# Performance work log

Hardware: AMD Instinct MI355X
Metric: run time of the kernel (lower is better)

The kernel has to match this reference:

```python
import jax, jax.numpy as jnp
import numpy as np

B=64; HW=14; E=2048; L=30; V=10000; EMB=512; AML=768; ADL=500
D=512+ADL   # decoder_dim + article_downlen = 1012
A=512+ADL   # attention_dim + article_downlen = 1012

def setup_inputs() -> dict:
    key = jax.random.key(0)
    ks = jax.random.split(key, 20)
    s = 0.02
    lin = lambda k, i, o: (jax.random.normal(k, (i, o), jnp.float32) * s)
    inp = {}
    inp['encoder_out'] = jax.random.normal(ks[0], (B, HW, HW, E), jnp.float32)
    inp['encoded_captions'] = jax.random.randint(ks[1], (B, L), 0, V)
    cl = jax.random.randint(ks[2], (B, 1), 2, L + 1)
    inp['caption_lengths'] = cl.at[0, 0].set(L)  # ensure max decode length == L-1
    inp['encoded_articles'] = jax.random.normal(ks[3], (B, 1, AML), jnp.float32)
    inp['article_lengths'] = jax.random.randint(ks[4], (B, 1), 1, AML)
    inp['blank_context'] = 0
    inp['E_emb'] = jax.random.uniform(ks[5], (V, EMB), jnp.float32, -0.1, 0.1)
    inp['W_par'] = lin(ks[6], AML, ADL); inp['b_par'] = jnp.zeros(ADL, jnp.float32)
    inp['W_enc'] = lin(ks[7], E, A);     inp['b_enc'] = jnp.zeros(A, jnp.float32)
    inp['W_dec'] = lin(ks[8], D, A);     inp['b_dec'] = jnp.zeros(A, jnp.float32)
    inp['W_full'] = lin(ks[9], A, 1);    inp['b_full'] = jnp.zeros(1, jnp.float32)
    inp['W_h'] = lin(ks[10], E + ADL, D); inp['b_h'] = jnp.zeros(D, jnp.float32)
    inp['W_c'] = lin(ks[11], E + ADL, D); inp['b_c'] = jnp.zeros(D, jnp.float32)
    inp['W_fb'] = lin(ks[12], D, E);      inp['b_fb'] = jnp.zeros(E, jnp.float32)
    inp['W_ih'] = lin(ks[13], EMB + E, 4 * D); inp['b_ih'] = jnp.zeros(4 * D, jnp.float32)
    inp['W_hh'] = lin(ks[14], D, 4 * D);       inp['b_hh'] = jnp.zeros(4 * D, jnp.float32)
    inp['W_fc'] = jax.random.uniform(ks[15], (D, V), jnp.float32, -0.1, 0.1)
    inp['b_fc'] = jnp.zeros(V, jnp.float32)
    return inp

def reference(encoder_out, encoded_captions, caption_lengths, encoded_articles,
              article_lengths, blank_context, E_emb, W_par, b_par, W_enc, b_enc,
              W_dec, b_dec, W_full, b_full, W_h, b_h, W_c, b_c, W_fb, b_fb,
              W_ih, b_ih, W_hh, b_hh, W_fc, b_fc):
    Bv = encoder_out.shape[0]
    enc = encoder_out.reshape(Bv, -1, encoder_out.shape[-1])  # (B, P, E)
    lens = caption_lengths[:, 0]
    sort_ind = jnp.argsort(-lens)
    lens = lens[sort_ind]
    enc = enc[sort_ind]
    caps = encoded_captions[sort_ind]
    arts = encoded_articles[sort_ind]
    emb = E_emb[caps]                                   # (B, L, EMB)
    context = (arts @ W_par + b_par)[:, 0, :]           # ParagraphEncoder -> (B, ADL)
    dec_in = jnp.concatenate([enc.mean(axis=1), context], axis=1)
    h0 = dec_in @ W_h + b_h
    c0 = dec_in @ W_c + b_c
    dlens = lens - 1
    att1 = enc @ W_enc + b_enc                          # loop-invariant, (B, P, A)
    T = emb.shape[1] - 1

    def step(carry, t):
        h, c = carry
        active = (dlens > t)[:, None]                   # prefix mask (sorted desc)
        att2 = h @ W_dec + b_dec
        scores = (jax.nn.relu(att1 + att2[:, None, :]) @ W_full)[..., 0] + b_full[0]
        alpha = jax.nn.softmax(scores, axis=1)          # (B, P)
        awe = jnp.einsum('bp,bpe->be', alpha, enc)
        awe = jax.nn.sigmoid(h @ W_fb + b_fb) * awe     # gated attention encoding
        x = jnp.concatenate([emb[:, t, :], awe], axis=1)
        gates = x @ W_ih + b_ih + h @ W_hh + b_hh       # torch LSTMCell, gate order i,f,g,o
        i, f, g, o = jnp.split(gates, 4, axis=1)
        c_new = jax.nn.sigmoid(f) * c + jax.nn.sigmoid(i) * jnp.tanh(g)
        h_new = jax.nn.sigmoid(o) * jnp.tanh(c_new)
        preds = jnp.where(active, h_new @ W_fc + b_fc, 0.0)
        alpha_m = jnp.where(active, alpha, 0.0)
        h = jnp.where(active, h_new, h)
        c = jnp.where(active, c_new, c)
        return (h, c), (preds, alpha_m)

    _, (preds, alphas) = jax.lax.scan(step, (h0, c0), jnp.arange(T))
    predictions = jnp.transpose(preds, (1, 0, 2))       # (B, T, V)
    alphas = jnp.transpose(alphas, (1, 0, 2))           # (B, T, P)
    return (predictions, caps, dlens, alphas, sort_ind)
```

## Files before the change

kernel.cpp:

```cpp
#include <hip/hip_runtime.h>
#include <math.h>

#define B_   64
#define P_   196
#define E_   2048
#define L_   30
#define T_   29
#define V_   10000
#define EMB_ 512
#define AML_ 768
#define ADL_ 500
#define D_   1012
#define A_   1012
#define G4_  4048
#define XK_  2560

typedef unsigned short u16;
typedef __attribute__((ext_vector_type(8))) short bf16x8;
typedef __attribute__((ext_vector_type(4))) float f32x4;

__device__ __forceinline__ float sigf(float x) { return 1.f / (1.f + __expf(-x)); }
__device__ __forceinline__ float tanhf_fast(float x) { return 1.f - 2.f / (__expf(2.f * x) + 1.f); }
__device__ __forceinline__ u16 f2bf(float f) {
    unsigned u = __float_as_uint(f);
    return (u16)((u + 0x7FFFu + ((u >> 16) & 1u)) >> 16);
}
__device__ __forceinline__ float bf2f(u16 v) { return __uint_as_float(((unsigned)v) << 16); }

__global__ void k_setup(const int* __restrict__ clen, const int* __restrict__ caps,
                        float* __restrict__ out_caps, float* __restrict__ out_dlens,
                        float* __restrict__ out_sind,
                        int* __restrict__ sort_ind, int* __restrict__ dlens_i,
                        int* __restrict__ nact, int* __restrict__ caps_s,
                        int* __restrict__ gcnt)
{
    __shared__ int lens[B_];
    int t = threadIdx.x;
    if (t < B_) lens[t] = clen[t];
    if (t < 64) gcnt[t] = 0;
    __syncthreads();
    if (t < B_) {
        int my = lens[t];
        int rank = 0;
        for (int j = 0; j < B_; ++j) {
            int lj = lens[j];
            if (lj > my || (lj == my && j < t)) rank++;
        }
        sort_ind[rank] = t;
    }
    __syncthreads();
    if (t < B_) {
        int orig = sort_ind[t];
        int dl = lens[orig] - 1;
        dlens_i[t] = dl;
        out_dlens[t] = (float)dl;
        out_sind[t] = (float)orig;
        for (int j = 0; j < L_; ++j) {
            int cv = caps[orig * L_ + j];
            caps_s[t * L_ + j] = cv;
            out_caps[t * L_ + j] = (float)cv;
        }
    }
    __syncthreads();
    if (t < T_) {
        int cnt = 0;
        for (int j = 0; j < B_; ++j) cnt += (dlens_i[j] > t) ? 1 : 0;
        nact[t] = cnt;
    }
}

__global__ void k_zero(float4* __restrict__ p, long n4)
{
    long i = (long)blockIdx.x * 256 + threadIdx.x;
    if (i < n4) p[i] = make_float4(0.f, 0.f, 0.f, 0.f);
}

__global__ void k_cvt_enc(const float* __restrict__ enc, const int* __restrict__ sort_ind,
                          u16* __restrict__ A_bf)
{
    int row = blockIdx.y;
    int b = row / 196, p = row - b * 196;
    int e4 = (blockIdx.x * 256 + threadIdx.x) * 4;
    const float* src = enc + ((long)sort_ind[b] * 196 + p) * E_ + e4;
    float4 v = *(const float4*)src;
    unsigned lo = (unsigned)f2bf(v.x) | ((unsigned)f2bf(v.y) << 16);
    unsigned hi = (unsigned)f2bf(v.z) | ((unsigned)f2bf(v.w) << 16);
    uint2 pk; pk.x = lo; pk.y = hi;
    *(uint2*)(A_bf + (long)row * E_ + e4) = pk;
}

__global__ void k_transpose(const float* __restrict__ src, u16* __restrict__ dst,
                            int K, int N, int Kp, int Np)
{
    __shared__ float tile[32][33];
    int n0 = blockIdx.x * 32, k0 = blockIdx.y * 32;
    int tx = threadIdx.x, ty = threadIdx.y;
    for (int r = ty; r < 32; r += 8) {
        int k = k0 + r, n = n0 + tx;
        tile[r][tx] = (k < K && n < N) ? src[(long)k * N + n] : 0.f;
    }
    __syncthreads();
    for (int r = ty; r < 32; r += 8) {
        int n = n0 + r, k = k0 + tx;
        if (n < Np && k < Kp) dst[(long)n * Kp + k] = f2bf(tile[tx][r]);
    }
}

__global__ void k_encmean(const float* __restrict__ enc, const int* __restrict__ sort_ind,
                          u16* __restrict__ dec_in)
{
    int b = blockIdx.y;
    int e = blockIdx.x * 256 + threadIdx.x;
    int orig = sort_ind[b];
    const float* src = enc + (long)orig * P_ * E_ + e;
    float s = 0.f;
    for (int p = 0; p < P_; ++p) s += src[(long)p * E_];
    dec_in[(long)b * XK_ + e] = f2bf(s * (1.f / 196.f));
}

__global__ void k_ctx(const float* __restrict__ arts, const float* __restrict__ W_par,
                      const float* __restrict__ b_par, const int* __restrict__ sort_ind,
                      u16* __restrict__ dec_in)
{
    int b = blockIdx.y;
    int k = blockIdx.x * 256 + threadIdx.x;
    if (k >= 512) return;
    float s = 0.f;
    if (k < ADL_) {
        int orig = sort_ind[b];
        const float* ar = arts + (long)orig * AML_;
        s = b_par[k];
        for (int m = 0; m < AML_; ++m) s = fmaf(ar[m], W_par[m * ADL_ + k], s);
    }
    dec_in[(long)b * XK_ + E_ + k] = f2bf(s);
}

__global__ void k_emb_all(const float* __restrict__ E_emb, const int* __restrict__ caps_s,
                          u16* __restrict__ emb_all)
{
    int t = blockIdx.x;
    int b = blockIdx.y;
    int tok = caps_s[b * L_ + t];
    for (int k = threadIdx.x; k < EMB_; k += 256)
        emb_all[((long)t * B_ + b) * EMB_ + k] = f2bf(E_emb[(long)tok * EMB_ + k]);
}

__global__ void __launch_bounds__(256) k_att1_mfma(
    const u16* __restrict__ A, const u16* __restrict__ W,
    const float* __restrict__ bias, u16* __restrict__ Yb)
{
    int w = threadIdx.x >> 6, lane = threadIdx.x & 63;
    int lr = lane & 15, lk = (lane >> 4) * 8;
    int n0 = blockIdx.x * 256 + w * 64;
    int r0 = blockIdx.y * 64;
    f32x4 acc[4][4];
#pragma unroll
    for (int i = 0; i < 4; ++i)
#pragma unroll
        for (int j = 0; j < 4; ++j) acc[i][j] = (f32x4){0.f, 0.f, 0.f, 0.f};
    const u16* ap = A + (long)(r0 + lr) * E_ + lk;
    const u16* wp = W + (long)(n0 + lr) * E_ + lk;
    for (int k = 0; k < E_; k += 32) {
        bf16x8 af[4], bf[4];
#pragma unroll
        for (int mt = 0; mt < 4; ++mt) af[mt] = *(const bf16x8*)(ap + (long)mt * 16 * E_ + k);
#pragma unroll
        for (int nt = 0; nt < 4; ++nt) bf[nt] = *(const bf16x8*)(wp + (long)nt * 16 * E_ + k);
#pragma unroll
        for (int mt = 0; mt < 4; ++mt)
#pragma unroll
            for (int nt = 0; nt < 4; ++nt)
                acc[mt][nt] = __builtin_amdgcn_mfma_f32_16x16x32_bf16(af[mt], bf[nt], acc[mt][nt], 0, 0, 0);
    }
#pragma unroll
    for (int mt = 0; mt < 4; ++mt) {
#pragma unroll
        for (int nt = 0; nt < 4; ++nt) {
            int n = n0 + nt * 16 + lr;
            float bv = (n < A_) ? bias[n] : 0.f;
#pragma unroll
            for (int j = 0; j < 4; ++j) {
                int row = r0 + mt * 16 + (lane >> 4) * 4 + j;
                u16 outv = (n < A_) ? f2bf(acc[mt][nt][j] + bv) : (u16)0;
                Yb[(long)row * 1024 + n] = outv;
            }
        }
    }
}

template <int ACT, int OUT, int PADZ>
__global__ void __launch_bounds__(256) k_skinny(
    const u16* __restrict__ A1, const u16* __restrict__ W1, int K1,
    const float* __restrict__ bias1, void* __restrict__ Yv,
    long ldY, long offY, int Nmax,
    const int* __restrict__ nact, int t)
{
    int Bact = (t >= 0) ? nact[t] : B_;
    if (Bact <= 0) return;
    int mmax = (Bact + 15) >> 4;
    int w = threadIdx.x >> 6, lane = threadIdx.x & 63;
    int lr = lane & 15, lk = (lane >> 4) * 8;
    int n0 = blockIdx.x * 64 + w * 16;
    f32x4 acc[4];
#pragma unroll
    for (int m = 0; m < 4; ++m) acc[m] = (f32x4){0.f, 0.f, 0.f, 0.f};

    int n = n0 + lr;
    int nc = n < Nmax ? n : Nmax - 1;
    const u16* a1p = A1 + (long)lr * K1 + lk;
    const u16* w1p = W1 + (long)nc * K1 + lk;
    for (int k = 0; k < K1; k += 32) {
        bf16x8 bw = *(const bf16x8*)(w1p + k);
#pragma unroll
        for (int m = 0; m < 4; ++m)
            if (m < mmax) {
                bf16x8 aw = *(const bf16x8*)(a1p + (long)m * 16 * K1 + k);
                acc[m] = __builtin_amdgcn_mfma_f32_16x16x32_bf16(aw, bw, acc[m], 0, 0, 0);
            }
    }
    float bv = (n < Nmax) ? bias1[n] : 0.f;
#pragma unroll
    for (int m = 0; m < 4; ++m) {
        if (m < mmax) {
#pragma unroll
            for (int j = 0; j < 4; ++j) {
                int b = m * 16 + (lane >> 4) * 4 + j;
                if (b < Bact) {
                    float v = acc[m][j] + bv;
                    if (ACT == 1) v = sigf(v);
                    if (n < Nmax) {
                        if (OUT == 1) ((u16*)Yv)[(long)b * ldY + offY + n] = f2bf(v);
                        else          ((float*)Yv)[(long)b * ldY + offY + n] = v;
                    } else if (PADZ) {
                        if (OUT == 1) ((u16*)Yv)[(long)b * ldY + offY + n] = 0;
                        else          ((float*)Yv)[(long)b * ldY + offY + n] = 0.f;
                    }
                }
            }
        }
    }
}

__global__ void __launch_bounds__(256) k_att2fb(
    const u16* __restrict__ h_bf, const u16* __restrict__ WT_dec,
    const u16* __restrict__ WT_fb, const float* __restrict__ b_dec,
    const float* __restrict__ b_fb, float* __restrict__ att2p,
    float* __restrict__ fbp, const int* __restrict__ nact, int t)
{
    int Bact = nact[t];
    if (Bact <= 0) return;
    int mmax = (Bact + 15) >> 4;
    int kh = blockIdx.x / 48;
    int nb = blockIdx.x - kh * 48;
    int isfb = nb >= 16;
    const u16* W = isfb ? WT_fb : WT_dec;
    const float* bias = isfb ? b_fb : b_dec;
    int Nmax = isfb ? E_ : A_;
    int nb2 = isfb ? nb - 16 : nb;
    long ldY = isfb ? (long)E_ : 1024L;
    float* Y = (isfb ? fbp : att2p) + (long)kh * B_ * ldY;

    int w = threadIdx.x >> 6, lane = threadIdx.x & 63;
    int lr = lane & 15, lk = (lane >> 4) * 8;
    int n = nb2 * 64 + w * 16 + lr;
    int nc = n < Nmax ? n : Nmax - 1;
    int k0 = kh * 256;
    f32x4 acc[4];
#pragma unroll
    for (int m = 0; m < 4; ++m) acc[m] = (f32x4){0.f, 0.f, 0.f, 0.f};
    const u16* ap = h_bf + (long)lr * 1024 + k0 + lk;
    const u16* wp = W + (long)nc * 1024 + k0 + lk;
    for (int k = 0; k < 256; k += 32) {
        bf16x8 bw = *(const bf16x8*)(wp + k);
#pragma unroll
        for (int m = 0; m < 4; ++m)
            if (m < mmax) {
                bf16x8 aw = *(const bf16x8*)(ap + (long)m * 16 * 1024 + k);
                acc[m] = __builtin_amdgcn_mfma_f32_16x16x32_bf16(aw, bw, acc[m], 0, 0, 0);
            }
    }
    if (n >= Nmax) return;
    float bv = (kh == 0) ? bias[n] : 0.f;
#pragma unroll
    for (int m = 0; m < 4; ++m) {
        if (m < mmax) {
#pragma unroll
            for (int j = 0; j < 4; ++j) {
                int b = m * 16 + (lane >> 4) * 4 + j;
                if (b < Bact) Y[(long)b * ldY + n] = acc[m][j] + bv;
            }
        }
    }
}

__global__ void k_scores(const u16* __restrict__ att1, const float* __restrict__ att2p,
                         const float* __restrict__ W_full, const float* __restrict__ b_full,
                         float* __restrict__ scores, const int* __restrict__ nact, int t)
{
    int b = blockIdx.y;
    if (b >= nact[t]) return;
    int wv = threadIdx.x >> 6;
    int lane = threadIdx.x & 63;
    int p = blockIdx.x * 4 + wv;
    const u16* a1 = att1 + ((long)b * P_ + p) * 1024;
    const float* a20 = att2p + (long)b * 1024;
    const float* a21 = a20 + 65536;
    const float* a22 = a20 + 131072;
    const float* a23 = a20 + 196608;
    float acc = 0.f;
    for (int j2 = lane; j2 < 506; j2 += 64) {
        unsigned pk = *(const unsigned*)(a1 + 2 * j2);
        float2 p0 = *(const float2*)(a20 + 2 * j2);
        float2 p1 = *(const float2*)(a21 + 2 * j2);
        float2 p2 = *(const float2*)(a22 + 2 * j2);
        float2 p3 = *(const float2*)(a23 + 2 * j2);
        float2 wv2 = *(const float2*)(W_full + 2 * j2);
        float v0 = bf2f((u16)(pk & 0xFFFF)) + p0.x + p1.x + p2.x + p3.x;
        float v1 = bf2f((u16)(pk >> 16)) + p0.y + p1.y + p2.y + p3.y;
        v0 = v0 > 0.f ? v0 : 0.f;
        v1 = v1 > 0.f ? v1 : 0.f;
        acc = fmaf(v0, wv2.x, acc);
        acc = fmaf(v1, wv2.y, acc);
    }
    for (int m = 32; m >= 1; m >>= 1) acc += __shfl_xor(acc, m);
    if (lane == 0) scores[b * P_ + p] = acc + b_full[0];
}

__global__ void __launch_bounds__(256) k_awe_x(
    const u16* __restrict__ A_bf, const float* __restrict__ scores,
    const float* __restrict__ fbp, u16* __restrict__ awe_buf,
    float* __restrict__ alphas_out, const int* __restrict__ nact, int t)
{
    int b = blockIdx.y;
    if (b >= nact[t]) return;
    int tid = threadIdx.x;
    int w = tid >> 6, lane = tid & 63;
    __shared__ float al[P_];
    __shared__ float red[4];
    float v = (tid < P_) ? scores[b * P_ + tid] : -1e30f;
    float m = v;
    for (int s = 32; s >= 1; s >>= 1) m = fmaxf(m, __shfl_xor(m, s));
    if (lane == 0) red[w] = m;
    __syncthreads();
    m = fmaxf(fmaxf(red[0], red[1]), fmaxf(red[2], red[3]));
    float e = (tid < P_) ? __expf(v - m) : 0.f;
    float s_ = e;
    for (int s = 32; s >= 1; s >>= 1) s_ += __shfl_xor(s_, s);
    __syncthreads();
    if (lane == 0) red[w] = s_;
    __syncthreads();
    s_ = red[0] + red[1] + red[2] + red[3];
    if (tid < P_) al[tid] = e / s_;
    __syncthreads();

    if (blockIdx.x < 8) {
        int e0 = blockIdx.x * 256 + tid;
        const u16* src = A_bf + (long)b * P_ * E_ + e0;
        float s0 = 0.f, s1 = 0.f, s2 = 0.f, s3 = 0.f;
        for (int p = 0; p < P_; p += 4) {
            s0 = fmaf(al[p],     bf2f(src[(long)p * E_]), s0);
            s1 = fmaf(al[p + 1], bf2f(src[(long)(p + 1) * E_]), s1);
            s2 = fmaf(al[p + 2], bf2f(src[(long)(p + 2) * E_]), s2);
            s3 = fmaf(al[p + 3], bf2f(src[(long)(p + 3) * E_]), s3);
        }
        long fb_off = (long)b * E_ + e0;
        float g = sigf(fbp[fb_off] + fbp[131072 + fb_off] + fbp[262144 + fb_off]
                       + fbp[393216 + fb_off]);
        awe_buf[(long)b * E_ + e0] = f2bf((s0 + s1 + s2 + s3) * g);
    } else {
        if (tid < P_) alphas_out[((long)b * T_ + t) * P_ + tid] = al[tid];
    }
}

__global__ void __launch_bounds__(256) k_gates_lstm3(
    const u16* __restrict__ emb_t, const u16* __restrict__ awe,
    const u16* __restrict__ h_old, const u16* __restrict__ WT_ih,
    const u16* __restrict__ WT_hh, const float* __restrict__ b_ih,
    const float* __restrict__ b_hh, float* __restrict__ gpart,
    int* __restrict__ gcnt, float* __restrict__ cbuf, u16* __restrict__ h_new,
    const int* __restrict__ nact, int t)
{
    int Bact = nact[t];
    if (Bact <= 0) return;
    int mmax = (Bact + 15) >> 4;
    int q = threadIdx.x >> 6;
    int lane = threadIdx.x & 63;
    int lr = lane & 15, lk = (lane >> 4) * 8;
    int nblk = blockIdx.x, kpart = blockIdx.y;
    int n = nblk * 16 + lr;
    int nc = n < D_ ? n : D_ - 1;
    f32x4 acc[4];
#pragma unroll
    for (int m = 0; m < 4; ++m) acc[m] = (f32x4){0.f, 0.f, 0.f, 0.f};
    const u16* wih = WT_ih + ((long)q * D_ + nc) * XK_;
    const u16* whh = WT_hh + ((long)q * D_ + nc) * 1024;

    const u16* ap; long astr; const u16* wp; int K;
    if (kpart == 0)      { ap = emb_t + (long)lr * EMB_ + lk;        astr = 16 * EMB_; wp = wih;        K = 512; }
    else if (kpart == 1) { ap = awe + (long)lr * E_ + lk;            astr = 16 * E_;   wp = wih + 512;  K = 1024; }
    else if (kpart == 2) { ap = awe + (long)lr * E_ + 1024 + lk;     astr = 16 * E_;   wp = wih + 1536; K = 1024; }
    else                 { ap = h_old + (long)lr * 1024 + lk;        astr = 16 * 1024; wp = whh;        K = 1024; }
    for (int k = 0; k < K; k += 32) {
        bf16x8 bw = *(const bf16x8*)(wp + k);
#pragma unroll
        for (int m = 0; m < 4; ++m)
            if (m < mmax) {
                bf16x8 aw = *(const bf16x8*)(ap + (long)m * astr + k);
                acc[m] = __builtin_amdgcn_mfma_f32_16x16x32_bf16(aw, bw, acc[m], 0, 0, 0);
            }
    }
#pragma unroll
    for (int m = 0; m < 4; ++m) {
        if (m < mmax) {
#pragma unroll
            for (int j = 0; j < 4; ++j) {
                int bb = m * 16 + (lane >> 4) * 4 + j;
                if (bb < Bact)
                    gpart[((long)kpart * B_ + bb) * 4096 + q * 1024 + n] = acc[m][j];
            }
        }
    }
    __threadfence();
    __syncthreads();
    __shared__ int isLast;
    if (threadIdx.x == 0) isLast = (atomicAdd(&gcnt[nblk], 1) == 3) ? 1 : 0;
    __syncthreads();
    if (!isLast) return;
    __threadfence();
#pragma unroll
    for (int i = 0; i < 4; ++i) {
        int idx = threadIdx.x + i * 256;
        int bb = idx >> 4, col = idx & 15;
        if (bb >= Bact) continue;
        int n2 = nblk * 16 + col;
        if (n2 >= D_) continue;
        const float* gp = gpart + (long)bb * 4096 + n2;
        float gi = gp[0]    + gp[262144]        + gp[524288]        + gp[786432]
                 + b_ih[n2]          + b_hh[n2];
        float gf = gp[1024] + gp[262144 + 1024] + gp[524288 + 1024] + gp[786432 + 1024]
                 + b_ih[D_ + n2]     + b_hh[D_ + n2];
        float gg = gp[2048] + gp[262144 + 2048] + gp[524288 + 2048] + gp[786432 + 2048]
                 + b_ih[2 * D_ + n2] + b_hh[2 * D_ + n2];
        float go = gp[3072] + gp[262144 + 3072] + gp[524288 + 3072] + gp[786432 + 3072]
                 + b_ih[3 * D_ + n2] + b_hh[3 * D_ + n2];
        float c = cbuf[(long)bb * 1024 + n2];
        float cn = sigf(gf) * c + sigf(gi) * tanhf_fast(gg);
        float hn = sigf(go) * tanhf_fast(cn);
        cbuf[(long)bb * 1024 + n2] = cn;
        h_new[(long)bb * 1024 + n2] = f2bf(hn);
    }
    if (threadIdx.x == 0) atomicExch(&gcnt[nblk], 0);
}

__global__ void __launch_bounds__(256) k_fc_all(
    const u16* __restrict__ h_all, const u16* __restrict__ W,
    const float* __restrict__ bias, float* __restrict__ out_preds,
    const int* __restrict__ nact)
{
    int tslot = blockIdx.y;
    int Bact = nact[tslot];
    if (Bact <= 0) return;
    int mmax = (Bact + 15) >> 4;
    int w = threadIdx.x >> 6, lane = threadIdx.x & 63;
    int lr = lane & 15, lk = (lane >> 4) * 8;
    int n0 = blockIdx.x * 256 + w * 64;
    f32x4 acc[4][4];
#pragma unroll
    for (int i = 0; i < 4; ++i)
#pragma unroll
        for (int j = 0; j < 4; ++j) acc[i][j] = (f32x4){0.f, 0.f, 0.f, 0.f};
    const u16* ap = h_all + ((long)(tslot + 1) * B_ + lr) * 1024 + lk;
    int ncl[4];
#pragma unroll
    for (int nt = 0; nt < 4; ++nt) {
        int n = n0 + nt * 16 + lr;
        ncl[nt] = n < V_ ? n : V_ - 1;
    }
    for (int k = 0; k < 1024; k += 32) {
        bf16x8 af[4], bf[4];
#pragma unroll
        for (int mt = 0; mt < 4; ++mt)
            if (mt < mmax) af[mt] = *(const bf16x8*)(ap + (long)mt * 16 * 1024 + k);
#pragma unroll
        for (int nt = 0; nt < 4; ++nt) bf[nt] = *(const bf16x8*)(W + (long)ncl[nt] * 1024 + lk + k);
#pragma unroll
        for (int mt = 0; mt < 4; ++mt)
            if (mt < mmax)
#pragma unroll
                for (int nt = 0; nt < 4; ++nt)
                    acc[mt][nt] = __builtin_amdgcn_mfma_f32_16x16x32_bf16(af[mt], bf[nt], acc[mt][nt], 0, 0, 0);
    }
#pragma unroll
    for (int nt = 0; nt < 4; ++nt) {
        int n = n0 + nt * 16 + lr;
        if (n >= V_) continue;
        float bv = bias[n];
#pragma unroll
        for (int mt = 0; mt < 4; ++mt) {
            if (mt < mmax) {
#pragma unroll
                for (int j = 0; j < 4; ++j) {
                    int b = mt * 16 + (lane >> 4) * 4 + j;
                    if (b < Bact)
                        out_preds[(long)b * T_ * V_ + (long)tslot * V_ + n] = acc[mt][nt][j] + bv;
                }
            }
        }
    }
}

extern "C" void kernel_launch(void* const* d_in, const int* in_sizes, int n_in,
                              void* d_out, int out_size, void* d_ws, size_t ws_size,
                              hipStream_t stream)
{
    const float* enc    = (const float*)d_in[0];
    const int*   caps   = (const int*)d_in[1];
    const int*   clen   = (const int*)d_in[2];
    const float* arts   = (const float*)d_in[3];
    const float* E_emb  = (const float*)d_in[6];
    const float* W_par  = (const float*)d_in[7];
    const float* b_par  = (const float*)d_in[8];
    const float* W_enc  = (const float*)d_in[9];
    const float* b_enc  = (const float*)d_in[10];
    const float* W_dec  = (const float*)d_in[11];
    const float* b_dec  = (const float*)d_in[12];
    const float* W_full = (const float*)d_in[13];
    const float* b_full = (const float*)d_in[14];
    const float* W_h    = (const float*)d_in[15];
    const float* b_h    = (const float*)d_in[16];
    const float* W_c    = (const float*)d_in[17];
    const float* b_c    = (const float*)d_in[18];
    const float* W_fb   = (const float*)d_in[19];
    const float* b_fb   = (const float*)d_in[20];
    const float* W_ih   = (const float*)d_in[21];
    const float* b_ih   = (const float*)d_in[22];
    const float* W_hh   = (const float*)d_in[23];
    const float* b_hh   = (const float*)d_in[24];
    const float* W_fc   = (const float*)d_in[25];
    const float* b_fc   = (const float*)d_in[26];

    float* out = (float*)d_out;
    float* out_preds  = out;
    float* out_caps   = out + (long)B_ * T_ * V_;
    float* out_dlens  = out_caps + B_ * L_;
    float* out_alphas = out_dlens + B_;
    float* out_sind   = out_alphas + (long)B_ * T_ * P_;

    float* ws = (float*)d_ws;
    long o = 0;
    auto alloc = [&](long n) { long r = o; o += (n + 63) & ~63L; return r; };
    long o_ints   = alloc(2240);
    long o_decin  = alloc((long)B_ * XK_ / 2);
    long o_hall   = alloc((long)(T_ + 1) * B_ * 1024 / 2);
    long o_emball = alloc((long)T_ * B_ * EMB_ / 2);
    long o_awe    = alloc((long)B_ * E_ / 2);
    long o_c      = alloc((long)B_ * 1024);
    long o_att2p  = alloc((long)4 * B_ * 1024);
    long o_fbp    = alloc((long)4 * B_ * 2048);
    long o_gpart  = alloc((long)4 * B_ * 4096);
    long o_scores = alloc((long)B_ * P_);
    long o_Abf    = alloc((long)12544 * E_ / 2);
    long o_att1   = alloc((long)12544 * 1024 / 2);
    long o_wtenc  = alloc((long)1024 * 2048 / 2);
    long o_wtdec  = alloc((long)1024 * 1024 / 2);
    long o_wtfb   = alloc((long)2048 * 1024 / 2);
    long o_wtih   = alloc((long)4096 * 2560 / 2);
    long o_wthh   = alloc((long)4096 * 1024 / 2);
    long o_wtfc   = alloc((long)10048 * 1024 / 2);

    int* sort_ind = (int*)(ws + o_ints);
    int* dlens_i  = sort_ind + 64;
    int* nact     = dlens_i + 64;
    int* caps_s   = nact + 32;
    int* gcnt     = caps_s + B_ * L_;
    u16*   dec_in  = (u16*)(ws + o_decin);
    u16*   h_all   = (u16*)(ws + o_hall);
    u16*   emb_all = (u16*)(ws + o_emball);
    u16*   awe_buf = (u16*)(ws + o_awe);
    float* cbuf   = ws + o_c;
    float* att2p  = ws + o_att2p;
    float* fbp    = ws + o_fbp;
    float* gpart  = ws + o_gpart;
    float* scores = ws + o_scores;
    u16*   A_bf   = (u16*)(ws + o_Abf);
    u16*   att1   = (u16*)(ws + o_att1);
    u16*   WT_enc = (u16*)(ws + o_wtenc);
    u16*   WT_dec = (u16*)(ws + o_wtdec);
    u16*   WT_fb  = (u16*)(ws + o_wtfb);
    u16*   WT_ih  = (u16*)(ws + o_wtih);
    u16*   WT_hh  = (u16*)(ws + o_wthh);
    u16*   WT_fc  = (u16*)(ws + o_wtfc);
    u16*   WT_h   = att1;
    u16*   WT_c   = att1 + (long)1024 * XK_;

    long n4 = ((long)B_ * T_ * V_ + B_ * L_ + B_ + (long)B_ * T_ * P_ + B_) / 4;
    k_zero<<<dim3((unsigned)((n4 + 255) / 256)), 256, 0, stream>>>((float4*)d_out, n4);
    k_setup<<<1, 64, 0, stream>>>(clen, caps, out_caps, out_dlens, out_sind,
                                  sort_ind, dlens_i, nact, caps_s, gcnt);

    k_encmean<<<dim3(8, 64), 256, 0, stream>>>(enc, sort_ind, dec_in);
    k_ctx<<<dim3(2, 64), 256, 0, stream>>>(arts, W_par, b_par, sort_ind, dec_in);
    k_emb_all<<<dim3(T_, 64), 256, 0, stream>>>(E_emb, caps_s, emb_all);

    dim3 tb(32, 8);
    k_transpose<<<dim3(1024/32, 2560/32), tb, 0, stream>>>(W_h, WT_h, 2548, 1012, 2560, 1024);
    k_transpose<<<dim3(1024/32, 2560/32), tb, 0, stream>>>(W_c, WT_c, 2548, 1012, 2560, 1024);
    k_skinny<0,1,1><<<dim3(16), 256, 0, stream>>>(dec_in, WT_h, XK_, b_h, h_all, 1024L, 0L, D_,
                                                  nact, -1);
    k_skinny<0,0,1><<<dim3(16), 256, 0, stream>>>(dec_in, WT_c, XK_, b_c, cbuf, 1024L, 0L, D_,
                                                  nact, -1);

    k_transpose<<<dim3(1024/32, 2048/32), tb, 0, stream>>>(W_enc, WT_enc, 2048, 1012, 2048, 1024);
    k_transpose<<<dim3(1024/32, 1024/32), tb, 0, stream>>>(W_dec, WT_dec, 1012, 1012, 1024, 1024);
    k_transpose<<<dim3(2048/32, 1024/32), tb, 0, stream>>>(W_fb, WT_fb, 1012, 2048, 1024, 2048);
    k_transpose<<<dim3(4096/32, 2560/32), tb, 0, stream>>>(W_ih, WT_ih, 2560, 4048, 2560, 4096);
    k_transpose<<<dim3(4096/32, 1024/32), tb, 0, stream>>>(W_hh, WT_hh, 1012, 4048, 1024, 4096);
    k_transpose<<<dim3(10048/32, 1024/32), tb, 0, stream>>>(W_fc, WT_fc, 1012, 10000, 1024, 10048);

    k_cvt_enc<<<dim3(2, 12544), 256, 0, stream>>>(enc, sort_ind, A_bf);
    k_att1_mfma<<<dim3(4, 196), 256, 0, stream>>>(A_bf, WT_enc, b_enc, att1);

    for (int t = 0; t < T_; ++t) {
        const u16* h_old = h_all + (long)t * B_ * 1024;
        u16* h_new = h_all + (long)(t + 1) * B_ * 1024;
        const u16* emb_t = emb_all + (long)t * B_ * EMB_;
        k_att2fb<<<dim3(192), 256, 0, stream>>>(h_old, WT_dec, WT_fb, b_dec, b_fb,
                                                att2p, fbp, nact, t);
        k_scores<<<dim3(49, 64), 256, 0, stream>>>(att1, att2p, W_full, b_full, scores, nact, t);
        k_awe_x<<<dim3(9, 64), 256, 0, stream>>>(A_bf, scores, fbp, awe_buf,
                                                 out_alphas, nact, t);
        k_gates_lstm3<<<dim3(64, 4), 256, 0, stream>>>(emb_t, awe_buf, h_old, WT_ih, WT_hh,
                                                       b_ih, b_hh, gpart, gcnt, cbuf, h_new,
                                                       nact, t);
    }
    k_fc_all<<<dim3(40, T_), 256, 0, stream>>>(h_all, WT_fc, b_fc, out_preds, nact);
}
```

Baseline: 3.196 ms.

## Precompute embedding gate GEMM, fuse scores with attention, stage att1 A in LDS

```diff
diff --git a/kernel.cpp b/kernel.cpp
--- a/kernel.cpp
+++ b/kernel.cpp
@@ -37,7 +37,7 @@
     __shared__ int lens[B_];
     int t = threadIdx.x;
     if (t < B_) lens[t] = clen[t];
-    if (t < 64) gcnt[t] = 0;
+    if (t < 64) { gcnt[t] = 0; gcnt[64 + t] = 0; }
     __syncthreads();
     if (t < B_) {
         int my = lens[t];
@@ -149,28 +149,42 @@
     const u16* __restrict__ A, const u16* __restrict__ W,
     const float* __restrict__ bias, u16* __restrict__ Yb)
 {
+    __shared__ u16 As[2][64][40];
     int w = threadIdx.x >> 6, lane = threadIdx.x & 63;
     int lr = lane & 15, lk = (lane >> 4) * 8;
     int n0 = blockIdx.x * 256 + w * 64;
     int r0 = blockIdx.y * 64;
+    int arow = threadIdx.x >> 2;
+    int akseg = (threadIdx.x & 3) * 8;
+    const u16* ag = A + (long)(r0 + arow) * E_ + akseg;
+
     f32x4 acc[4][4];
 #pragma unroll
     for (int i = 0; i < 4; ++i)
 #pragma unroll
         for (int j = 0; j < 4; ++j) acc[i][j] = (f32x4){0.f, 0.f, 0.f, 0.f};
-    const u16* ap = A + (long)(r0 + lr) * E_ + lk;
     const u16* wp = W + (long)(n0 + lr) * E_ + lk;
+
+    *(uint2*)&As[0][arow][akseg] = *(const uint2*)(ag);
+    __syncthreads();
+
     for (int k = 0; k < E_; k += 32) {
-        bf16x8 af[4], bf[4];
-#pragma unroll
-        for (int mt = 0; mt < 4; ++mt) af[mt] = *(const bf16x8*)(ap + (long)mt * 16 * E_ + k);
+        int buf = (k >> 5) & 1;
+        bool more = (k + 32) < E_;
+        uint2 pre;
+        if (more) pre = *(const uint2*)(ag + k + 32);
+        bf16x8 bf[4], af[4];
 #pragma unroll
         for (int nt = 0; nt < 4; ++nt) bf[nt] = *(const bf16x8*)(wp + (long)nt * 16 * E_ + k);
+#pragma unroll
+        for (int mt = 0; mt < 4; ++mt) af[mt] = *(const bf16x8*)&As[buf][mt * 16 + lr][lk];
 #pragma unroll
         for (int mt = 0; mt < 4; ++mt)
 #pragma unroll
             for (int nt = 0; nt < 4; ++nt)
                 acc[mt][nt] = __builtin_amdgcn_mfma_f32_16x16x32_bf16(af[mt], bf[nt], acc[mt][nt], 0, 0, 0);
+        if (more) *(uint2*)&As[buf ^ 1][arow][akseg] = pre;
+        __syncthreads();
     }
 #pragma unroll
     for (int mt = 0; mt < 4; ++mt) {
@@ -241,6 +255,53 @@
     }
 }
 
+__global__ void __launch_bounds__(256) k_gemb(
+    const u16* __restrict__ emb_all, const u16* __restrict__ WT_ih,
+    float* __restrict__ gemb_all)
+{
+    int t = blockIdx.y;
+    int w = threadIdx.x >> 6, lane = threadIdx.x & 63;
+    int lr = lane & 15, lk = (lane >> 4) * 8;
+    int n0 = blockIdx.x * 256 + w * 64;
+    f32x4 acc[4][4];
+#pragma unroll
+    for (int i = 0; i < 4; ++i)
+#pragma unroll
+        for (int j = 0; j < 4; ++j) acc[i][j] = (f32x4){0.f, 0.f, 0.f, 0.f};
+    const u16* ap = emb_all + ((long)t * B_ + lr) * EMB_ + lk;
+    long wrow[4];
+#pragma unroll
+    for (int nt = 0; nt < 4; ++nt) {
+        int j = n0 + nt * 16 + lr;
+        int q = j >> 10, d = j & 1023;
+        wrow[nt] = (long)q * D_ + (d < D_ ? d : D_ - 1);
+    }
+    for (int k = 0; k < EMB_; k += 32) {
+        bf16x8 af[4], bf[4];
+#pragma unroll
+        for (int mt = 0; mt < 4; ++mt) af[mt] = *(const bf16x8*)(ap + (long)mt * 16 * EMB_ + k);
+#pragma unroll
+        for (int nt = 0; nt < 4; ++nt) bf[nt] = *(const bf16x8*)(WT_ih + wrow[nt] * XK_ + lk + k);
+#pragma unroll
+        for (int mt = 0; mt < 4; ++mt)
+#pragma unroll
+            for (int nt = 0; nt < 4; ++nt)
+                acc[mt][nt] = __builtin_amdgcn_mfma_f32_16x16x32_bf16(af[mt], bf[nt], acc[mt][nt], 0, 0, 0);
+    }
+#pragma unroll
+    for (int nt = 0; nt < 4; ++nt) {
+        int j = n0 + nt * 16 + lr;
+#pragma unroll
+        for (int mt = 0; mt < 4; ++mt) {
+#pragma unroll
+            for (int jj = 0; jj < 4; ++jj) {
+                int b = mt * 16 + (lane >> 4) * 4 + jj;
+                gemb_all[((long)t * B_ + b) * 4096 + j] = acc[mt][nt][jj];
+            }
+        }
+    }
+}
+
 __global__ void __launch_bounds__(256) k_att2fb(
     const u16* __restrict__ h_bf, const u16* __restrict__ WT_dec,
     const u16* __restrict__ WT_fb, const float* __restrict__ b_dec,
@@ -293,48 +354,51 @@
     }
 }
 
-__global__ void k_scores(const u16* __restrict__ att1, const float* __restrict__ att2p,
-                         const float* __restrict__ W_full, const float* __restrict__ b_full,
-                         float* __restrict__ scores, const int* __restrict__ nact, int t)
-{
-    int b = blockIdx.y;
-    if (b >= nact[t]) return;
-    int wv = threadIdx.x >> 6;
-    int lane = threadIdx.x & 63;
-    int p = blockIdx.x * 4 + wv;
-    const u16* a1 = att1 + ((long)b * P_ + p) * 1024;
-    const float* a20 = att2p + (long)b * 1024;
-    const float* a21 = a20 + 65536;
-    const float* a22 = a20 + 131072;
-    const float* a23 = a20 + 196608;
-    float acc = 0.f;
-    for (int j2 = lane; j2 < 506; j2 += 64) {
-        unsigned pk = *(const unsigned*)(a1 + 2 * j2);
-        float2 p0 = *(const float2*)(a20 + 2 * j2);
-        float2 p1 = *(const float2*)(a21 + 2 * j2);
-        float2 p2 = *(const float2*)(a22 + 2 * j2);
-        float2 p3 = *(const float2*)(a23 + 2 * j2);
-        float2 wv2 = *(const float2*)(W_full + 2 * j2);
-        float v0 = bf2f((u16)(pk & 0xFFFF)) + p0.x + p1.x + p2.x + p3.x;
-        float v1 = bf2f((u16)(pk >> 16)) + p0.y + p1.y + p2.y + p3.y;
-        v0 = v0 > 0.f ? v0 : 0.f;
-        v1 = v1 > 0.f ? v1 : 0.f;
-        acc = fmaf(v0, wv2.x, acc);
-        acc = fmaf(v1, wv2.y, acc);
-    }
-    for (int m = 32; m >= 1; m >>= 1) acc += __shfl_xor(acc, m);
-    if (lane == 0) scores[b * P_ + p] = acc + b_full[0];
-}
-
-__global__ void __launch_bounds__(256) k_awe_x(
-    const u16* __restrict__ A_bf, const float* __restrict__ scores,
-    const float* __restrict__ fbp, u16* __restrict__ awe_buf,
-    float* __restrict__ alphas_out, const int* __restrict__ nact, int t)
+__global__ void __launch_bounds__(256) k_attn(
+    const u16* __restrict__ att1, const float* __restrict__ att2p,
+    const float* __restrict__ W_full, const float* __restrict__ b_full,
+    const u16* __restrict__ A_bf, const float* __restrict__ fbp,
+    float* __restrict__ scores, u16* __restrict__ awe_buf,
+    float* __restrict__ alphas_out, int* __restrict__ gcnt2,
+    const int* __restrict__ nact, int t)
 {
     int b = blockIdx.y;
     if (b >= nact[t]) return;
     int tid = threadIdx.x;
     int w = tid >> 6, lane = tid & 63;
+    {
+        int p = blockIdx.x * 4 + w;
+        const u16* a1 = att1 + ((long)b * P_ + p) * 1024;
+        const float* a20 = att2p + (long)b * 1024;
+        const float* a21 = a20 + 65536;
+        const float* a22 = a20 + 131072;
+        const float* a23 = a20 + 196608;
+        float acc = 0.f;
+        for (int j2 = lane; j2 < 506; j2 += 64) {
+            unsigned pk = *(const unsigned*)(a1 + 2 * j2);
+            float2 p0 = *(const float2*)(a20 + 2 * j2);
+            float2 p1 = *(const float2*)(a21 + 2 * j2);
+            float2 p2 = *(const float2*)(a22 + 2 * j2);
+            float2 p3 = *(const float2*)(a23 + 2 * j2);
+            float2 wv2 = *(const float2*)(W_full + 2 * j2);
+            float v0 = bf2f((u16)(pk & 0xFFFF)) + p0.x + p1.x + p2.x + p3.x;
+            float v1 = bf2f((u16)(pk >> 16)) + p0.y + p1.y + p2.y + p3.y;
+            v0 = v0 > 0.f ? v0 : 0.f;
+            v1 = v1 > 0.f ? v1 : 0.f;
+            acc = fmaf(v0, wv2.x, acc);
+            acc = fmaf(v1, wv2.y, acc);
+        }
+        for (int m = 32; m >= 1; m >>= 1) acc += __shfl_xor(acc, m);
+        if (lane == 0) scores[b * P_ + p] = acc + b_full[0];
+    }
+    __threadfence();
+    __syncthreads();
+    __shared__ int isLast;
+    if (tid == 0) isLast = (atomicAdd(&gcnt2[b], 1) == 48) ? 1 : 0;
+    __syncthreads();
+    if (!isLast) return;
+    __threadfence();
+
     __shared__ float al[P_];
     __shared__ float red[4];
     float v = (tid < P_) ? scores[b * P_ + tid] : -1e30f;
@@ -350,32 +414,39 @@
     if (lane == 0) red[w] = s_;
     __syncthreads();
     s_ = red[0] + red[1] + red[2] + red[3];
-    if (tid < P_) al[tid] = e / s_;
-    __syncthreads();
-
-    if (blockIdx.x < 8) {
-        int e0 = blockIdx.x * 256 + tid;
-        const u16* src = A_bf + (long)b * P_ * E_ + e0;
-        float s0 = 0.f, s1 = 0.f, s2 = 0.f, s3 = 0.f;
-        for (int p = 0; p < P_; p += 4) {
-            s0 = fmaf(al[p],     bf2f(src[(long)p * E_]), s0);
-            s1 = fmaf(al[p + 1], bf2f(src[(long)(p + 1) * E_]), s1);
-            s2 = fmaf(al[p + 2], bf2f(src[(long)(p + 2) * E_]), s2);
-            s3 = fmaf(al[p + 3], bf2f(src[(long)(p + 3) * E_]), s3);
-        }
-        long fb_off = (long)b * E_ + e0;
+    if (tid < P_) {
+        float a = e / s_;
+        al[tid] = a;
+        alphas_out[((long)b * T_ + t) * P_ + tid] = a;
+    }
+    __syncthreads();
+
+    int e0 = tid * 8;
+    const u16* src = A_bf + (long)b * P_ * E_ + e0;
+    float s0[8];
+#pragma unroll
+    for (int j = 0; j < 8; ++j) s0[j] = 0.f;
+    for (int p2 = 0; p2 < P_; ++p2) {
+        float a = al[p2];
+        bf16x8 vv = *(const bf16x8*)(src + (long)p2 * E_);
+#pragma unroll
+        for (int j = 0; j < 8; ++j) s0[j] = fmaf(a, bf2f((u16)vv[j]), s0[j]);
+    }
+#pragma unroll
+    for (int j = 0; j < 8; ++j) {
+        int e2 = e0 + j;
+        long fb_off = (long)b * E_ + e2;
         float g = sigf(fbp[fb_off] + fbp[131072 + fb_off] + fbp[262144 + fb_off]
                        + fbp[393216 + fb_off]);
-        awe_buf[(long)b * E_ + e0] = f2bf((s0 + s1 + s2 + s3) * g);
-    } else {
-        if (tid < P_) alphas_out[((long)b * T_ + t) * P_ + tid] = al[tid];
-    }
+        awe_buf[(long)b * E_ + e2] = f2bf(s0[j] * g);
+    }
+    if (tid == 0) atomicExch(&gcnt2[b], 0);
 }
 
 __global__ void __launch_bounds__(256) k_gates_lstm3(
-    const u16* __restrict__ emb_t, const u16* __restrict__ awe,
-    const u16* __restrict__ h_old, const u16* __restrict__ WT_ih,
-    const u16* __restrict__ WT_hh, const float* __restrict__ b_ih,
+    const u16* __restrict__ awe, const u16* __restrict__ h_old,
+    const u16* __restrict__ WT_ih, const u16* __restrict__ WT_hh,
+    const float* __restrict__ gemb_t, const float* __restrict__ b_ih,
     const float* __restrict__ b_hh, float* __restrict__ gpart,
     int* __restrict__ gcnt, float* __restrict__ cbuf, u16* __restrict__ h_new,
     const int* __restrict__ nact, int t)
@@ -395,12 +466,11 @@
     const u16* wih = WT_ih + ((long)q * D_ + nc) * XK_;
     const u16* whh = WT_hh + ((long)q * D_ + nc) * 1024;
 
-    const u16* ap; long astr; const u16* wp; int K;
-    if (kpart == 0)      { ap = emb_t + (long)lr * EMB_ + lk;        astr = 16 * EMB_; wp = wih;        K = 512; }
-    else if (kpart == 1) { ap = awe + (long)lr * E_ + lk;            astr = 16 * E_;   wp = wih + 512;  K = 1024; }
-    else if (kpart == 2) { ap = awe + (long)lr * E_ + 1024 + lk;     astr = 16 * E_;   wp = wih + 1536; K = 1024; }
-    else                 { ap = h_old + (long)lr * 1024 + lk;        astr = 16 * 1024; wp = whh;        K = 1024; }
-    for (int k = 0; k < K; k += 32) {
+    const u16* ap; long astr; const u16* wp;
+    if (kpart == 0)      { ap = awe + (long)lr * E_ + lk;          astr = 16 * E_;   wp = wih + 512;  }
+    else if (kpart == 1) { ap = awe + (long)lr * E_ + 1024 + lk;   astr = 16 * E_;   wp = wih + 1536; }
+    else                 { ap = h_old + (long)lr * 1024 + lk;      astr = 16 * 1024; wp = whh;        }
+    for (int k = 0; k < 1024; k += 32) {
         bf16x8 bw = *(const bf16x8*)(wp + k);
 #pragma unroll
         for (int m = 0; m < 4; ++m)
@@ -423,7 +493,7 @@
     __threadfence();
     __syncthreads();
     __shared__ int isLast;
-    if (threadIdx.x == 0) isLast = (atomicAdd(&gcnt[nblk], 1) == 3) ? 1 : 0;
+    if (threadIdx.x == 0) isLast = (atomicAdd(&gcnt[nblk], 1) == 2) ? 1 : 0;
     __syncthreads();
     if (!isLast) return;
     __threadfence();
@@ -435,13 +505,14 @@
         int n2 = nblk * 16 + col;
         if (n2 >= D_) continue;
         const float* gp = gpart + (long)bb * 4096 + n2;
-        float gi = gp[0]    + gp[262144]        + gp[524288]        + gp[786432]
+        const float* ge = gemb_t + (long)bb * 4096 + n2;
+        float gi = gp[0]    + gp[262144]        + gp[524288]        + ge[0]
                  + b_ih[n2]          + b_hh[n2];
-        float gf = gp[1024] + gp[262144 + 1024] + gp[524288 + 1024] + gp[786432 + 1024]
+        float gf = gp[1024] + gp[262144 + 1024] + gp[524288 + 1024] + ge[1024]
                  + b_ih[D_ + n2]     + b_hh[D_ + n2];
-        float gg = gp[2048] + gp[262144 + 2048] + gp[524288 + 2048] + gp[786432 + 2048]
+        float gg = gp[2048] + gp[262144 + 2048] + gp[524288 + 2048] + ge[2048]
                  + b_ih[2 * D_ + n2] + b_hh[2 * D_ + n2];
-        float go = gp[3072] + gp[262144 + 3072] + gp[524288 + 3072] + gp[786432 + 3072]
+        float go = gp[3072] + gp[262144 + 3072] + gp[524288 + 3072] + ge[3072]
                  + b_ih[3 * D_ + n2] + b_hh[3 * D_ + n2];
         float c = cbuf[(long)bb * 1024 + n2];
         float cn = sigf(gf) * c + sigf(gi) * tanhf_fast(gg);
@@ -549,7 +620,7 @@
     float* ws = (float*)d_ws;
     long o = 0;
     auto alloc = [&](long n) { long r = o; o += (n + 63) & ~63L; return r; };
-    long o_ints   = alloc(2240);
+    long o_ints   = alloc(2304);
     long o_decin  = alloc((long)B_ * XK_ / 2);
     long o_hall   = alloc((long)(T_ + 1) * B_ * 1024 / 2);
     long o_emball = alloc((long)T_ * B_ * EMB_ / 2);
@@ -557,7 +628,8 @@
     long o_c      = alloc((long)B_ * 1024);
     long o_att2p  = alloc((long)4 * B_ * 1024);
     long o_fbp    = alloc((long)4 * B_ * 2048);
-    long o_gpart  = alloc((long)4 * B_ * 4096);
+    long o_gpart  = alloc((long)3 * B_ * 4096);
+    long o_gemb   = alloc((long)T_ * B_ * 4096);
     long o_scores = alloc((long)B_ * P_);
     long o_Abf    = alloc((long)12544 * E_ / 2);
     long o_att1   = alloc((long)12544 * 1024 / 2);
@@ -573,6 +645,7 @@
     int* nact     = dlens_i + 64;
     int* caps_s   = nact + 32;
     int* gcnt     = caps_s + B_ * L_;
+    int* gcnt2    = gcnt + 64;
     u16*   dec_in  = (u16*)(ws + o_decin);
     u16*   h_all   = (u16*)(ws + o_hall);
     u16*   emb_all = (u16*)(ws + o_emball);
@@ -581,6 +654,7 @@
     float* att2p  = ws + o_att2p;
     float* fbp    = ws + o_fbp;
     float* gpart  = ws + o_gpart;
+    float* gemb_all = ws + o_gemb;
     float* scores = ws + o_scores;
     u16*   A_bf   = (u16*)(ws + o_Abf);
     u16*   att1   = (u16*)(ws + o_att1);
@@ -619,17 +693,17 @@
 
     k_cvt_enc<<<dim3(2, 12544), 256, 0, stream>>>(enc, sort_ind, A_bf);
     k_att1_mfma<<<dim3(4, 196), 256, 0, stream>>>(A_bf, WT_enc, b_enc, att1);
+    k_gemb<<<dim3(16, T_), 256, 0, stream>>>(emb_all, WT_ih, gemb_all);
 
     for (int t = 0; t < T_; ++t) {
         const u16* h_old = h_all + (long)t * B_ * 1024;
         u16* h_new = h_all + (long)(t + 1) * B_ * 1024;
-        const u16* emb_t = emb_all + (long)t * B_ * EMB_;
+        const float* gemb_t = gemb_all + (long)t * B_ * 4096;
         k_att2fb<<<dim3(192), 256, 0, stream>>>(h_old, WT_dec, WT_fb, b_dec, b_fb,
                                                 att2p, fbp, nact, t);
-        k_scores<<<dim3(49, 64), 256, 0, stream>>>(att1, att2p, W_full, b_full, scores, nact, t);
-        k_awe_x<<<dim3(9, 64), 256, 0, stream>>>(A_bf, scores, fbp, awe_buf,
-                                                 out_alphas, nact, t);
-        k_gates_lstm3<<<dim3(64, 4), 256, 0, stream>>>(emb_t, awe_buf, h_old, WT_ih, WT_hh,
+        k_attn<<<dim3(49, 64), 256, 0, stream>>>(att1, att2p, W_full, b_full, A_bf, fbp,
+                                                 scores, awe_buf, out_alphas, gcnt2, nact, t);
+        k_gates_lstm3<<<dim3(64, 3), 256, 0, stream>>>(awe_buf, h_old, WT_ih, WT_hh, gemb_t,
                                                        b_ih, b_hh, gpart, gcnt, cbuf, h_new,
                                                        nact, t);
     }
```

Result: slower. 7.807 ms (+144.3%).
